# Kernel tuning notes

Measured on AMD Instinct MI355X. Metric: run time of the kernel, lower is better.

Reference implementation:

```python
import jax, jax.numpy as jnp
import numpy as np

NEG = -1000000.0  # mask fill value used by the torch module


def setup_inputs() -> dict:
    key = jax.random.key(0)
    kq, kk, kv, km = jax.random.split(key, 4)
    B, Q, K, D = 8, 2048, 2048, 128
    queries = jax.random.normal(kq, (B, Q, D), dtype=jnp.float32)
    keys = jax.random.normal(kk, (B, K, D), dtype=jnp.float32)
    values = jax.random.normal(kv, (B, K, D), dtype=jnp.float32)
    attntion_mask = jax.random.randint(km, (B, K), 0, 2, dtype=jnp.int32)
    return {"queries": queries, "keys": keys, "values": values,
            "attntion_mask": attntion_mask}


def reference(queries, keys, values, attntion_mask):
    d = queries.shape[-1]
    # scores: [B, Q, K]
    scores = jnp.einsum('bqd,bkd->bqk', queries, keys) / jnp.sqrt(
        jnp.asarray(d, dtype=queries.dtype))
    # 2D mask [B, K] broadcasts over the query axis (torch repeat_interleave)
    mask = attntion_mask.astype(bool)[:, None, :]  # [B, 1, K]
    scores = jnp.where(mask, scores, NEG)
    weights = jax.nn.softmax(scores, axis=-1)
    # dropout rate is 0.0 (eval mode) -> identity
    return jnp.einsum('bqk,bkv->bqv', weights, values)
```

## Files before the change

### kernel.cpp

```cpp
#include <hip/hip_runtime.h>
#include <stdint.h>

typedef __attribute__((ext_vector_type(8))) short short8;
typedef __attribute__((ext_vector_type(4))) float f32x4;

#define NB 8
#define NQ 2048
#define NK 2048
#define ND 128
#define SCALE 0.08838834764831845f
#define L2E   1.4426950408889634f
#define FMAXC 10.0f

__device__ __forceinline__ uint32_t pk_bf16(float a, float b) {
  uint32_t ua = __builtin_bit_cast(uint32_t, a);
  uint32_t ub = __builtin_bit_cast(uint32_t, b);
  ua += 0x7FFFu + ((ua >> 16) & 1u);
  ub += 0x7FFFu + ((ub >> 16) & 1u);
  return (ua >> 16) | (ub & 0xFFFF0000u);
}

__device__ __forceinline__ void dma16(const void* g, void* l) {
  __builtin_amdgcn_global_load_lds((const __attribute__((address_space(1))) void*)g,
                                   (__attribute__((address_space(3))) void*)l, 16, 0, 0);
}

__global__ __launch_bounds__(256) void compact_kernel(const int* __restrict__ maskm,
                                                      int* __restrict__ idxArr,
                                                      int* __restrict__ KcArr) {
  __shared__ int cnt;
  const int b = blockIdx.x;
  const int t = threadIdx.x;
  const int lane = t & 63;
  if (t == 0) cnt = 0;
  __syncthreads();
#pragma unroll
  for (int j = 0; j < 8; ++j) {
    int k = t * 8 + j;
    bool bit = maskm[b * NK + k] != 0;
    unsigned long long m = __ballot(bit);
    int pre = __popcll(m & ((1ull << lane) - 1ull));
    int tot = __popcll(m);
    int base = 0;
    if (lane == 0 && tot) base = atomicAdd(&cnt, tot);
    base = __shfl(base, 0);
    if (bit) idxArr[b * NK + base + pre] = k;
  }
  __syncthreads();
  int kc = cnt;
  for (int s = kc + t; s < NK; s += 256) idxArr[b * NK + s] = -1;
  if (t == 0) KcArr[b] = kc;
}

__global__ __launch_bounds__(256) void prep_kernel(const float* __restrict__ v,
                                                   const float* __restrict__ kin,
                                                   ushort* __restrict__ vt,
                                                   ushort* __restrict__ kb,
                                                   const int* __restrict__ idxArr) {
  const int t = threadIdx.x;
  const int bid = blockIdx.x;
  if (bid < 512) {
    __shared__ __align__(16) float tile[4096];
    char* sm = (char*)tile;
    const int b = bid >> 6;
    const int k0 = ((bid >> 1) & 31) << 6;
    const int d0 = (bid & 1) << 6;
#pragma unroll
    for (int i = 0; i < 4; ++i) {
      int id = i * 256 + t;
      int k = id >> 4, c = id & 15;
      int src = idxArr[b * NK + k0 + k];
      uint4 val; val.x = 0u; val.y = 0u; val.z = 0u; val.w = 0u;
      if (src >= 0) val = *(const uint4*)(v + (size_t)(b * NK + src) * ND + d0 + c * 4);
      *(uint4*)(sm + k * 256 + ((c ^ (k & 15)) * 16)) = val;
    }
    __syncthreads();
#pragma unroll
    for (int i = 0; i < 2; ++i) {
      int id = i * 256 + t;
      int d = id >> 3, kc = id & 7;
      uint32_t w[4];
#pragma unroll
      for (int jj = 0; jj < 4; ++jj) {
        int kA = kc * 8 + jj * 2, kB = kA + 1;
        float fa = *(const float*)(sm + kA * 256 + (((d >> 2) ^ (kA & 15)) * 16) + (d & 3) * 4);
        float fb = *(const float*)(sm + kB * 256 + (((d >> 2) ^ (kB & 15)) * 16) + (d & 3) * 4);
        w[jj] = pk_bf16(fa, fb);
      }
      uint4 o; o.x = w[0]; o.y = w[1]; o.z = w[2]; o.w = w[3];
      *(uint4*)(vt + (size_t)(b * ND + d0 + d) * NK + k0 + kc * 8) = o;
    }
  } else {
    int gs = (bid - 512) * 16 + (t >> 4);
    int src = idxArr[gs];
    int col = (t & 15) * 8;
    uint4 u; u.x = 0u; u.y = 0u; u.z = 0u; u.w = 0u;
    if (src >= 0) {
      int b2 = gs >> 11;
      const float* p = kin + (size_t)(b2 * NK + src) * ND + col;
      f32x4 a = *(const f32x4*)p;
      f32x4 c = *(const f32x4*)(p + 4);
      u.x = pk_bf16(a[0], a[1]); u.y = pk_bf16(a[2], a[3]);
      u.z = pk_bf16(c[0], c[1]); u.w = pk_bf16(c[2], c[3]);
    }
    *(uint4*)(kb + (size_t)gs * ND + col) = u;
  }
}

template <bool MASKED>
__device__ __forceinline__ void do_softmax(const f32x4 st[2], float& l_,
                                           char* pbase, int r, int quad, int rem) {
  const float C1 = SCALE * L2E;
  const float C2 = -FMAXC * L2E;
  float p[2][4]; float ps = 0.f;
#pragma unroll
  for (int mt = 0; mt < 2; ++mt) {
    float t0 = fmaf(st[mt][0], C1, C2);
    float t1 = fmaf(st[mt][1], C1, C2);
    float t2 = fmaf(st[mt][2], C1, C2);
    float t3 = fmaf(st[mt][3], C1, C2);
    if (MASKED) {
      const int rm = rem - mt * 16;
      t0 = (rm > 0) ? t0 : -2.0e6f;
      t1 = (rm > 1) ? t1 : -2.0e6f;
      t2 = (rm > 2) ? t2 : -2.0e6f;
      t3 = (rm > 3) ? t3 : -2.0e6f;
    }
    p[mt][0] = exp2f(t0); p[mt][1] = exp2f(t1);
    p[mt][2] = exp2f(t2); p[mt][3] = exp2f(t3);
    ps += p[mt][0] + p[mt][1] + p[mt][2] + p[mt][3];
  }
  l_ += ps;
#pragma unroll
  for (int mt = 0; mt < 2; ++mt) {
    uint2 w; w.x = pk_bf16(p[mt][0], p[mt][1]); w.y = pk_bf16(p[mt][2], p[mt][3]);
    *(uint2*)(pbase + r * 64 + (((mt * 4 + quad) ^ (r & 6)) * 8)) = w;
  }
}

#define LDS_BYTES 69632
__global__ __launch_bounds__(256) void attn_kernel(const float* __restrict__ qm,
                                                   const ushort* __restrict__ kbm,
                                                   const ushort* __restrict__ vtm,
                                                   const int* __restrict__ KcArr,
                                                   float* __restrict__ outm) {
  __shared__ __align__(16) char sm[LDS_BYTES];
  const int o   = blockIdx.x;
  const int bid = (o & 7) * 64 + (o >> 3);
  const int b   = bid >> 6;
  const int q0  = (bid & 63) << 5;
  const int t = threadIdx.x;
  const int lane = t & 63;
  const int wave = t >> 6;
  const int r = lane & 15;
  const int quad = lane >> 4;
  const int qg = wave >> 1;
  const int kq = wave & 1;

  const int Kc   = KcArr[b];
  const int n_it = (Kc + 63) >> 6;
  const int CH   = n_it << 5;

  uint32_t koff[4], voff[4];
#pragma unroll
  for (int j = 0; j < 4; ++j) {
    int i = wave * 4 + j;
    int rho = i * 4 + (lane >> 4);
    int ck = (lane & 15) ^ (rho & 15);
    koff[j] = (uint32_t)(b * NK + (rho >> 5) * CH + (rho & 31)) * ND + ck * 8;
    int u = i * 16 + (lane >> 2);
    int cv = (lane & 3) ^ (u & 3);
    voff[j] = (uint32_t)(b * ND + (u & 127)) * NK + (u >> 7) * CH + cv * 8;
  }

#define ISSUE_K(tt, bufi)                                                       \
  {                                                                             \
    const uint32_t kadd_ = (uint32_t)(tt) * 32 * ND;                            \
    char* kb_ = sm + (bufi) * 16384;                                            \
    _Pragma("unroll")                                                           \
    for (int j = 0; j < 4; ++j)                                                 \
      dma16(kbm + koff[j] + kadd_, kb_ + (wave * 4 + j) * 1024);                \
  }
#define ISSUE_V(tt)                                                             \
  {                                                                             \
    const uint32_t vadd_ = (uint32_t)(tt) * 32;                                 \
    _Pragma("unroll")                                                           \
    for (int j = 0; j < 4; ++j)                                                 \
      dma16(vtm + voff[j] + vadd_, sm + 49152 + (wave * 4 + j) * 1024);         \
  }

  f32x4 qraw[4][2];
#pragma unroll
  for (int ks = 0; ks < 4; ++ks) {
    const float* p = qm + (size_t)(b * NQ + q0 + qg * 16 + r) * ND + ks * 32 + quad * 8;
    qraw[ks][0] = *(const f32x4*)p;
    qraw[ks][1] = *(const f32x4*)(p + 4);
  }
  ISSUE_K(0, 0);
  if (n_it > 1) ISSUE_K(1, 1);
  short8 qf[4];
#pragma unroll
  for (int ks = 0; ks < 4; ++ks) {
    uint4 u;
    u.x = pk_bf16(qraw[ks][0][0], qraw[ks][0][1]);
    u.y = pk_bf16(qraw[ks][0][2], qraw[ks][0][3]);
    u.z = pk_bf16(qraw[ks][1][0], qraw[ks][1][1]);
    u.w = pk_bf16(qraw[ks][1][2], qraw[ks][1][3]);
    qf[ks] = __builtin_bit_cast(short8, u);
  }

  f32x4 oacc[8];
#pragma unroll
  for (int dt = 0; dt < 8; ++dt) oacc[dt] = (f32x4){0.f, 0.f, 0.f, 0.f};
  float l_ = 0.f;

  char* const pbase = sm + 65536 + wave * 1024;
  char* const vbuf  = sm + 49152 + kq * 8192;

  const int vlim0 = Kc - kq * CH;

  int cur = 0;
  for (int it = 0; it < n_it; ++it) {
    if (it + 1 < n_it) asm volatile("s_waitcnt vmcnt(4)" ::: "memory");
    else               asm volatile("s_waitcnt vmcnt(0)" ::: "memory");
    __builtin_amdgcn_sched_barrier(0);
    __builtin_amdgcn_s_barrier();
    __builtin_amdgcn_sched_barrier(0);

    ISSUE_V(it);
    if (it + 2 < n_it) {
      int b2 = cur + 2; if (b2 >= 3) b2 -= 3;
      ISSUE_K(it + 2, b2);
    }

    char* const kcur = sm + cur * 16384 + kq * 8192;

    f32x4 st[2];
#pragma unroll
    for (int mt = 0; mt < 2; ++mt) {
      short8 kf[4];
#pragma unroll
      for (int ks = 0; ks < 4; ++ks)
        kf[ks] = *(const short8*)(kcur + (mt * 16 + r) * 256 + (((ks * 4 + quad) ^ r) * 16));
      f32x4 acc = (f32x4){0.f, 0.f, 0.f, 0.f};
#pragma unroll
      for (int ks = 0; ks < 4; ++ks)
        acc = __builtin_amdgcn_mfma_f32_16x16x32_bf16(kf[ks], qf[ks], acc, 0, 0, 0);
      st[mt] = acc;
    }

    const int vlim = vlim0 - it * 32;
    if (vlim >= 32) do_softmax<false>(st, l_, pbase, r, quad, 0);
    else            do_softmax<true >(st, l_, pbase, r, quad, vlim - quad * 4);
    short8 pf = *(const short8*)(pbase + r * 64 + (((quad * 2) ^ (r & 6)) * 8));

    if (it + 2 < n_it) asm volatile("s_waitcnt vmcnt(4)" ::: "memory");
    else               asm volatile("s_waitcnt vmcnt(0)" ::: "memory");
    __builtin_amdgcn_sched_barrier(0);
    __builtin_amdgcn_s_barrier();
    __builtin_amdgcn_sched_barrier(0);

#pragma unroll
    for (int dt = 0; dt < 8; ++dt) {
      short8 vf = *(const short8*)(vbuf + (dt * 16 + r) * 64 + ((quad ^ (r & 3)) * 16));
      oacc[dt] = __builtin_amdgcn_mfma_f32_16x16x32_bf16(vf, pf, oacc[dt], 0, 0, 0);
    }

    cur = (cur == 2) ? 0 : cur + 1;
  }

  __syncthreads();
  float* xch = (float*)(sm + qg * 9216) + lane * 36;
  if (kq == 1) {
    xch[0] = l_;
#pragma unroll
    for (int dt = 0; dt < 8; ++dt)
      *(f32x4*)(xch + 4 + dt * 4) = oacc[dt];
  }
  __syncthreads();
  if (kq == 0) {
    const int qrow = b * NQ + q0 + qg * 16 + r;
    float ls = l_ + xch[0];
    ls += __shfl_xor(ls, 16);
    ls += __shfl_xor(ls, 32);
    float inv = 1.0f / ls;
#pragma unroll
    for (int dt = 0; dt < 8; ++dt) {
      f32x4 o1 = *(const f32x4*)(xch + 4 + dt * 4);
      f32x4 ov = oacc[dt];
      ov[0] = (ov[0] + o1[0]) * inv;
      ov[1] = (ov[1] + o1[1]) * inv;
      ov[2] = (ov[2] + o1[2]) * inv;
      ov[3] = (ov[3] + o1[3]) * inv;
      *(f32x4*)(outm + (size_t)qrow * ND + dt * 16 + quad * 4) = ov;
    }
  }
#undef ISSUE_K
#undef ISSUE_V
}

extern "C" void kernel_launch(void* const* d_in, const int* in_sizes, int n_in,
                              void* d_out, int out_size, void* d_ws, size_t ws_size,
                              hipStream_t stream) {
  const float* q   = (const float*)d_in[0];
  const float* k   = (const float*)d_in[1];
  const float* v   = (const float*)d_in[2];
  const int*   msk = (const int*)d_in[3];
  float* out = (float*)d_out;
  ushort* kb = (ushort*)d_ws;
  ushort* vt = kb + (size_t)NB * NK * ND;
  int* idxA  = (int*)(vt + (size_t)NB * NK * ND);
  int* kcA   = idxA + (size_t)NB * NK;

  compact_kernel<<<NB, 256, 0, stream>>>(msk, idxA, kcA);
  prep_kernel<<<1536, 256, 0, stream>>>(v, k, vt, kb, idxA);
  attn_kernel<<<512, 256, 0, stream>>>(q, kb, vt, kcA, out);
}
```

Before: 105.0 us.

## Triple-buffer K and V tiles together, use 512-thread attention blocks

The attention kernel now prefetches K and V tiles together into a three-deep LDS ring. That lets it drop the second per-iteration barrier and wait that used to guard the V buffer. Blocks grow to 8 waves covering 64 query rows, with half as many blocks and each wave issuing half as many DMA loads per tile. The K-conversion part of the prep kernel processes 128 rows per block in an unrolled loop, shrinking its grid. The cost is more LDS per block and fewer blocks in flight, which may reduce latency hiding or occupancy.

```diff
diff --git a/kernel.cpp b/kernel.cpp
--- a/kernel.cpp
+++ b/kernel.cpp
@@ -91,19 +91,23 @@
       *(uint4*)(vt + (size_t)(b * ND + d0 + d) * NK + k0 + kc * 8) = o;
     }
   } else {
-    int gs = (bid - 512) * 16 + (t >> 4);
-    int src = idxArr[gs];
-    int col = (t & 15) * 8;
-    uint4 u; u.x = 0u; u.y = 0u; u.z = 0u; u.w = 0u;
-    if (src >= 0) {
-      int b2 = gs >> 11;
-      const float* p = kin + (size_t)(b2 * NK + src) * ND + col;
-      f32x4 a = *(const f32x4*)p;
-      f32x4 c = *(const f32x4*)(p + 4);
-      u.x = pk_bf16(a[0], a[1]); u.y = pk_bf16(a[2], a[3]);
-      u.z = pk_bf16(c[0], c[1]); u.w = pk_bf16(c[2], c[3]);
-    }
-    *(uint4*)(kb + (size_t)gs * ND + col) = u;
+    const int kblk = bid - 512;
+#pragma unroll
+    for (int pass = 0; pass < 8; ++pass) {
+      int gs = kblk * 128 + pass * 16 + (t >> 4);
+      int src = idxArr[gs];
+      int col = (t & 15) * 8;
+      uint4 u; u.x = 0u; u.y = 0u; u.z = 0u; u.w = 0u;
+      if (src >= 0) {
+        int b2 = gs >> 11;
+        const float* p = kin + (size_t)(b2 * NK + src) * ND + col;
+        f32x4 a = *(const f32x4*)p;
+        f32x4 c = *(const f32x4*)(p + 4);
+        u.x = pk_bf16(a[0], a[1]); u.y = pk_bf16(a[2], a[3]);
+        u.z = pk_bf16(c[0], c[1]); u.w = pk_bf16(c[2], c[3]);
+      }
+      *(uint4*)(kb + (size_t)gs * ND + col) = u;
+    }
   }
 }
 
@@ -138,17 +142,17 @@
   }
 }
 
-#define LDS_BYTES 69632
-__global__ __launch_bounds__(256) void attn_kernel(const float* __restrict__ qm,
+#define LDS_BYTES 106496
+__global__ __launch_bounds__(512) void attn_kernel(const float* __restrict__ qm,
                                                    const ushort* __restrict__ kbm,
                                                    const ushort* __restrict__ vtm,
                                                    const int* __restrict__ KcArr,
                                                    float* __restrict__ outm) {
   __shared__ __align__(16) char sm[LDS_BYTES];
   const int o   = blockIdx.x;
-  const int bid = (o & 7) * 64 + (o >> 3);
-  const int b   = bid >> 6;
-  const int q0  = (bid & 63) << 5;
+  const int bid = (o & 7) * 32 + (o >> 3);
+  const int b   = bid >> 5;
+  const int q0  = (bid & 31) << 6;
   const int t = threadIdx.x;
   const int lane = t & 63;
   const int wave = t >> 6;
@@ -161,10 +165,10 @@
   const int n_it = (Kc + 63) >> 6;
   const int CH   = n_it << 5;
 
-  uint32_t koff[4], voff[4];
-#pragma unroll
-  for (int j = 0; j < 4; ++j) {
-    int i = wave * 4 + j;
+  uint32_t koff[2], voff[2];
+#pragma unroll
+  for (int j = 0; j < 2; ++j) {
+    int i = wave * 2 + j;
     int rho = i * 4 + (lane >> 4);
     int ck = (lane & 15) ^ (rho & 15);
     koff[j] = (uint32_t)(b * NK + (rho >> 5) * CH + (rho & 31)) * ND + ck * 8;
@@ -173,20 +177,17 @@
     voff[j] = (uint32_t)(b * ND + (u & 127)) * NK + (u >> 7) * CH + cv * 8;
   }
 
-#define ISSUE_K(tt, bufi)                                                       \
+#define ISSUE_TILE(tt, bufi)                                                    \
   {                                                                             \
     const uint32_t kadd_ = (uint32_t)(tt) * 32 * ND;                            \
+    const uint32_t vadd_ = (uint32_t)(tt) * 32;                                 \
     char* kb_ = sm + (bufi) * 16384;                                            \
+    char* vb_ = sm + 49152 + (bufi) * 16384;                                    \
     _Pragma("unroll")                                                           \
-    for (int j = 0; j < 4; ++j)                                                 \
-      dma16(kbm + koff[j] + kadd_, kb_ + (wave * 4 + j) * 1024);                \
-  }
-#define ISSUE_V(tt)                                                             \
-  {                                                                             \
-    const uint32_t vadd_ = (uint32_t)(tt) * 32;                                 \
-    _Pragma("unroll")                                                           \
-    for (int j = 0; j < 4; ++j)                                                 \
-      dma16(vtm + voff[j] + vadd_, sm + 49152 + (wave * 4 + j) * 1024);         \
+    for (int j = 0; j < 2; ++j) {                                               \
+      dma16(kbm + koff[j] + kadd_, kb_ + (wave * 2 + j) * 1024);                \
+      dma16(vtm + voff[j] + vadd_, vb_ + (wave * 2 + j) * 1024);                \
+    }                                                                           \
   }
 
   f32x4 qraw[4][2];
@@ -196,8 +197,8 @@
     qraw[ks][0] = *(const f32x4*)p;
     qraw[ks][1] = *(const f32x4*)(p + 4);
   }
-  ISSUE_K(0, 0);
-  if (n_it > 1) ISSUE_K(1, 1);
+  ISSUE_TILE(0, 0);
+  if (n_it > 1) ISSUE_TILE(1, 1);
   short8 qf[4];
 #pragma unroll
   for (int ks = 0; ks < 4; ++ks) {
@@ -214,8 +215,7 @@
   for (int dt = 0; dt < 8; ++dt) oacc[dt] = (f32x4){0.f, 0.f, 0.f, 0.f};
   float l_ = 0.f;
 
-  char* const pbase = sm + 65536 + wave * 1024;
-  char* const vbuf  = sm + 49152 + kq * 8192;
+  char* const pbase = sm + 98304 + wave * 1024;
 
   const int vlim0 = Kc - kq * CH;
 
@@ -227,13 +227,13 @@
     __builtin_amdgcn_s_barrier();
     __builtin_amdgcn_sched_barrier(0);
 
-    ISSUE_V(it);
     if (it + 2 < n_it) {
       int b2 = cur + 2; if (b2 >= 3) b2 -= 3;
-      ISSUE_K(it + 2, b2);
+      ISSUE_TILE(it + 2, b2);
     }
 
     char* const kcur = sm + cur * 16384 + kq * 8192;
+    char* const vcur = sm + 49152 + cur * 16384 + kq * 8192;
 
     f32x4 st[2];
 #pragma unroll
@@ -254,15 +254,9 @@
     else            do_softmax<true >(st, l_, pbase, r, quad, vlim - quad * 4);
     short8 pf = *(const short8*)(pbase + r * 64 + (((quad * 2) ^ (r & 6)) * 8));
 
-    if (it + 2 < n_it) asm volatile("s_waitcnt vmcnt(4)" ::: "memory");
-    else               asm volatile("s_waitcnt vmcnt(0)" ::: "memory");
-    __builtin_amdgcn_sched_barrier(0);
-    __builtin_amdgcn_s_barrier();
-    __builtin_amdgcn_sched_barrier(0);
-
 #pragma unroll
     for (int dt = 0; dt < 8; ++dt) {
-      short8 vf = *(const short8*)(vbuf + (dt * 16 + r) * 64 + ((quad ^ (r & 3)) * 16));
+      short8 vf = *(const short8*)(vcur + (dt * 16 + r) * 64 + ((quad ^ (r & 3)) * 16));
       oacc[dt] = __builtin_amdgcn_mfma_f32_16x16x32_bf16(vf, pf, oacc[dt], 0, 0, 0);
     }
 
@@ -295,8 +289,7 @@
       *(f32x4*)(outm + (size_t)qrow * ND + dt * 16 + quad * 4) = ov;
     }
   }
-#undef ISSUE_K
-#undef ISSUE_V
+#undef ISSUE_TILE
 }
 
 extern "C" void kernel_launch(void* const* d_in, const int* in_sizes, int n_in,
@@ -313,6 +306,6 @@
   int* kcA   = idxA + (size_t)NB * NK;
 
   compact_kernel<<<NB, 256, 0, stream>>>(msk, idxA, kcA);
-  prep_kernel<<<1536, 256, 0, stream>>>(v, k, vt, kb, idxA);
-  attn_kernel<<<512, 256, 0, stream>>>(q, kb, vt, kcA, out);
-}
+  prep_kernel<<<640, 256, 0, stream>>>(v, k, vt, kb, idxA);
+  attn_kernel<<<256, 512, 0, stream>>>(q, kb, vt, kcA, out);
+}
```

Result: slower. 107.2 us (+2.1%).
